# Kernel optimization log

Hardware: AMD Instinct MI355X
Metric: run time of the kernel (lower is better)

## Reference

```python
import jax, jax.numpy as jnp
import numpy as np

B, T, C, H = 2, 2048, 1024, 16
HD = C // H  # head dim = 64


def setup_inputs() -> dict:
    key = jax.random.key(0)
    ks = jax.random.split(key, 5)
    s = 0.02  # GPT-style init scale for weights
    return {
        "x": jax.random.normal(ks[0], (B, T, C), dtype=jnp.float32),
        "Wq": jax.random.normal(ks[1], (C, C), dtype=jnp.float32) * s,
        "bq": jnp.zeros((C,), dtype=jnp.float32),
        "Wk": jax.random.normal(ks[2], (C, C), dtype=jnp.float32) * s,
        "bk": jnp.zeros((C,), dtype=jnp.float32),
        "Wv": jax.random.normal(ks[3], (C, C), dtype=jnp.float32) * s,
        "bv": jnp.zeros((C,), dtype=jnp.float32),
        "Wp": jax.random.normal(ks[4], (C, C), dtype=jnp.float32) * s,
        "bp": jnp.zeros((C,), dtype=jnp.float32),
    }


def reference(x, Wq, bq, Wk, bk, Wv, bv, Wp, bp):
    b, t, c = x.shape
    # torch nn.Linear: y = x @ W.T + b  (W is [out, in])
    def heads(W, bias):
        y = jnp.einsum("btc,oc->bto", x, W) + bias
        return y.reshape(b, t, H, HD).transpose(0, 2, 1, 3)  # [B,H,T,hd]

    q = heads(Wq, bq)
    k = heads(Wk, bk)
    v = heads(Wv, bv)

    scale = 1.0 / np.sqrt(HD).astype(np.float32)
    att = jnp.einsum("bhqd,bhkd->bhqk", q, k) * scale  # [B,H,T,T]
    causal = jnp.tril(jnp.ones((t, t), dtype=bool))
    att = jnp.where(causal[None, None], att, -jnp.inf)
    att = jax.nn.softmax(att, axis=-1)
    # attn_pdrop = 0.0 -> dropout is identity
    y = jnp.einsum("bhqk,bhkd->bhqd", att, v)  # [B,H,T,hd]
    y = y.transpose(0, 2, 1, 3).reshape(b, t, c)
    y = jnp.einsum("btc,oc->bto", y, Wp) + bp  # resid_pdrop = 0.0
    return y
```

## Files before the change

kernel.cpp:

```cpp
#include <hip/hip_runtime.h>
#include <hip/hip_bf16.h>

using bf16 = __hip_bfloat16;
typedef __attribute__((ext_vector_type(8))) short short8;
typedef __attribute__((ext_vector_type(4))) float floatx4;

#define B_  2
#define T_  2048
#define C_  1024
#define H_  16
#define HD_ 64
#define BT_ (B_*T_)
#define NX_ ((size_t)BT_*C_)
#define NW_ ((size_t)C_*C_)
#define PSTR2 40
#define KSCQ 0.1803368801f

__device__ __forceinline__ void gl2lds16(const bf16* g, bf16* l) {
    __builtin_amdgcn_global_load_lds((const __attribute__((address_space(1))) unsigned int*)g,
                                     (__attribute__((address_space(3))) unsigned int*)l,
                                     16, 0, 0);
}

__global__ __launch_bounds__(256) void cvt_f32_bf16(
    const float* __restrict__ x,
    const float* __restrict__ Wq, const float* __restrict__ Wk,
    const float* __restrict__ Wv, const float* __restrict__ Wp,
    bf16* __restrict__ xb, bf16* __restrict__ wqb, bf16* __restrict__ wkb,
    bf16* __restrict__ wvb, bf16* __restrict__ wpb)
{
    size_t i4 = ((size_t)blockIdx.x * 256 + threadIdx.x) * 4;
    const float* src; bf16* dst; size_t off;
    if (i4 < NX_) { src = x; dst = xb; off = i4; }
    else {
        size_t j = i4 - NX_;
        int r = (int)(j >> 20);
        off = j & (NW_ - 1);
        src = (r==0) ? Wq : (r==1) ? Wk : (r==2) ? Wv : Wp;
        dst = (r==0) ? wqb : (r==1) ? wkb : (r==2) ? wvb : wpb;
    }
    float4 v = *(const float4*)(src + off);
    union { bf16 h[4]; uint2 u; } o;
    o.h[0] = __float2bfloat16(v.x); o.h[1] = __float2bfloat16(v.y);
    o.h[2] = __float2bfloat16(v.z); o.h[3] = __float2bfloat16(v.w);
    *(uint2*)(dst + off) = o.u;
}

__global__ __launch_bounds__(256) void qkv_gemm(
    const bf16* __restrict__ x,
    const bf16* __restrict__ Wq, const float* __restrict__ bq,
    const bf16* __restrict__ Wk, const float* __restrict__ bk,
    const bf16* __restrict__ Wv, const float* __restrict__ bv,
    bf16* __restrict__ qo, bf16* __restrict__ ko, bf16* __restrict__ vt)
{
    __shared__ __align__(16) bf16 As[128*32];
    __shared__ __align__(16) bf16 Bs[128*32];

    const int tid  = threadIdx.x;
    const int w    = tid >> 6, lane = tid & 63;
    const int g    = lane >> 4, c16 = lane & 15;
    const int wr   = w >> 1,    wc  = w & 1;
    const int mtile = blockIdx.x, ntile = blockIdx.y;
    const int wsel  = ntile >> 3;
    const bf16*  W    = (wsel==0) ? Wq : (wsel==1 ? Wk : Wv);
    const float* bias = (wsel==0) ? bq : (wsel==1 ? bk : bv);
    const float oscale = (wsel==0) ? KSCQ : 1.0f;
    const int nbase  = (ntile & 7) * 128;

    const bf16* ag = x + (size_t)(mtile*128)*C_;
    const bf16* bg = W + (size_t)nbase*C_;

    floatx4 acc[4][4] = {};

    for (int k0 = 0; k0 < C_; k0 += 32) {
        #pragma unroll
        for (int p = 0; p < 2; ++p) {
            int cb = p*256 + w*64;
            int c  = cb + lane;
            gl2lds16(ag + (size_t)(c>>2)*C_ + k0 + (c&3)*8, As + cb*8);
            gl2lds16(bg + (size_t)(c>>2)*C_ + k0 + (c&3)*8, Bs + cb*8);
        }
        __syncthreads();

        short8 af[4], bfr[4];
        #pragma unroll
        for (int i = 0; i < 4; ++i)
            af[i] = *(const short8*)(As + (wr*64 + i*16 + c16)*32 + g*8);
        #pragma unroll
        for (int j = 0; j < 4; ++j)
            bfr[j] = *(const short8*)(Bs + (wc*64 + j*16 + c16)*32 + g*8);
        #pragma unroll
        for (int i = 0; i < 4; ++i)
            #pragma unroll
            for (int j = 0; j < 4; ++j)
                acc[i][j] = __builtin_amdgcn_mfma_f32_16x16x32_bf16(af[i], bfr[j], acc[i][j], 0, 0, 0);
        __syncthreads();
    }

    #pragma unroll
    for (int i = 0; i < 4; ++i) {
        int m0 = mtile*128 + wr*64 + i*16 + g*4;
        #pragma unroll
        for (int j = 0; j < 4; ++j) {
            int n = nbase + wc*64 + j*16 + c16;
            float bvf = bias[n];
            if (wsel == 2) {
                int bb = m0 >> 11, t0 = m0 & (T_-1);
                int hh = n >> 6,  hd = n & 63;
                union { bf16 hv[4]; uint2 u; } tmp;
                #pragma unroll
                for (int r = 0; r < 4; ++r) tmp.hv[r] = __float2bfloat16(acc[i][j][r] + bvf);
                *(uint2*)(vt + ((size_t)((bb*H_ + hh)*64 + hd))*T_ + t0) = tmp.u;
            } else {
                bf16* dst = (wsel==0) ? qo : ko;
                #pragma unroll
                for (int r = 0; r < 4; ++r)
                    dst[(size_t)(m0+r)*C_ + n] = __float2bfloat16((acc[i][j][r] + bvf) * oscale);
            }
        }
    }
}

__global__ __launch_bounds__(512, 4) void attn(
    const bf16* __restrict__ q, const bf16* __restrict__ k,
    const bf16* __restrict__ vt, bf16* __restrict__ y)
{
    __shared__ __align__(16) bf16 Ks[16*512];
    __shared__ __align__(16) bf16 Vs[16*512];
    __shared__ __align__(16) bf16 Ps[8][16*PSTR2];

    const int tid = threadIdx.x, w = tid >> 6, lane = tid & 63;
    const int g = lane >> 4, c16 = lane & 15;
    const int wq = w & 3;
    const int kh = w >> 2;

    const int xcd = blockIdx.x & 7;
    const int j   = blockIdx.x >> 3;
    const int p   = j & 15;
    const int bh  = (j >> 4) * 8 + xcd;
    const int b = bh >> 4, h = bh & 15;

    const bf16* kbase = k  + ((size_t)(b*T_))*C_ + h*64;
    const bf16* vbase = vt + ((size_t)(b*H_ + h))*64*T_;

    const short ONEB = 0x3F80;
    const short8 ones = {ONEB,ONEB,ONEB,ONEB,ONEB,ONEB,ONEB,ONEB};

    for (int ph = 0; ph < 2; ++ph) {
        const int qt = ph ? 31 - p : p;
        const int qbase = qt*64 + wq*16;
        const int nit = (qt + 2) >> 1;
        const int qglob = qbase + c16;

        short8 aq[2];
        #pragma unroll
        for (int kg = 0; kg < 2; ++kg)
            aq[kg] = *(const short8*)(q + ((size_t)(b*T_ + qglob))*C_ + h*64 + kg*32 + g*8);

        floatx4 accO[4] = {};
        floatx4 lacc = {};

        for (int kt = 0; kt < nit; ++kt) {
            #pragma unroll
            for (int e = 0; e < 2; ++e) {
                int f = w*2 + e;
                gl2lds16(kbase + (size_t)(kt*128 + (f>>1)*16 + c16)*C_ + (f&1)*32 + g*8, Ks + f*512);
                gl2lds16(vbase + (size_t)((f&3)*16 + c16)*T_ + kt*128 + (f>>2)*32 + g*8, Vs + f*512);
            }
            __syncthreads();

            floatx4 s[4];
            #pragma unroll
            for (int ct = 0; ct < 4; ++ct) {
                int ce = kh*4 + ct;
                short8 kb0 = *(const short8*)(Ks + (ce*2+0)*512 + lane*8);
                short8 kb1 = *(const short8*)(Ks + (ce*2+1)*512 + lane*8);
                floatx4 a = {0.f, 0.f, 0.f, 0.f};
                a = __builtin_amdgcn_mfma_f32_16x16x32_bf16(kb0, aq[0], a, 0, 0, 0);
                a = __builtin_amdgcn_mfma_f32_16x16x32_bf16(kb1, aq[1], a, 0, 0, 0);
                s[ct] = a;
            }

            if (kt == nit-1) {
                #pragma unroll
                for (int ct = 0; ct < 4; ++ct)
                    #pragma unroll
                    for (int r = 0; r < 4; ++r) {
                        int key = kt*128 + kh*64 + ct*16 + g*4 + r;
                        if (key > qglob) s[ct][r] = -1e30f;
                    }
            }

            #pragma unroll
            for (int ks = 0; ks < 2; ++ks) {
                #pragma unroll
                for (int half = 0; half < 2; ++half) {
                    int ct = ks*2 + half;
                    float p0 = exp2f(s[ct][0]);
                    float p1 = exp2f(s[ct][1]);
                    float p2 = exp2f(s[ct][2]);
                    float p3 = exp2f(s[ct][3]);
                    union { __hip_bfloat162 h2[2]; uint2 u; } pk;
                    pk.h2[0] = __float22bfloat162_rn(float2{p0, p1});
                    pk.h2[1] = __float22bfloat162_rn(float2{p2, p3});
                    *(uint2*)(Ps[w] + c16*PSTR2 + half*16 + g*4) = pk.u;
                }
                short8 pa = *(const short8*)(Ps[w] + c16*PSTR2 + g*8);
                lacc = __builtin_amdgcn_mfma_f32_16x16x32_bf16(pa, ones, lacc, 0, 0, 0);
                #pragma unroll
                for (int nt = 0; nt < 4; ++nt) {
                    short8 vb = *(const short8*)(Vs + ((kh*2 + ks)*4 + nt)*512 + lane*8);
                    accO[nt] = __builtin_amdgcn_mfma_f32_16x16x32_bf16(pa, vb, accO[nt], 0, 0, 0);
                }
            }
            __syncthreads();
        }

        if (w >= 4) {
            float* dstf = ((w < 6) ? (float*)Ks : (float*)Vs) + (w & 1)*1280 + lane*20;
            #pragma unroll
            for (int nt = 0; nt < 4; ++nt) *(floatx4*)(dstf + nt*4) = accO[nt];
            *(floatx4*)(dstf + 16) = lacc;
        }
        __syncthreads();
        if (w < 4) {
            int pw = w + 4;
            const float* srcf = ((pw < 6) ? (const float*)Ks : (const float*)Vs) + (pw & 1)*1280 + lane*20;
            #pragma unroll
            for (int nt = 0; nt < 4; ++nt) {
                floatx4 o = *(const floatx4*)(srcf + nt*4);
                #pragma unroll
                for (int r = 0; r < 4; ++r) accO[nt][r] += o[r];
            }
            floatx4 lo = *(const floatx4*)(srcf + 16);
            #pragma unroll
            for (int r = 0; r < 4; ++r) lacc[r] += lo[r];

            float ir[4];
            #pragma unroll
            for (int r = 0; r < 4; ++r) ir[r] = __builtin_amdgcn_rcpf(lacc[r]);
            #pragma unroll
            for (int nt = 0; nt < 4; ++nt)
                #pragma unroll
                for (int r = 0; r < 4; ++r) {
                    int row = qbase + g*4 + r;
                    float o = accO[nt][r] * ir[r];
                    y[((size_t)(b*T_ + row))*C_ + h*64 + nt*16 + c16] = __float2bfloat16(o);
                }
        }
        __syncthreads();
    }
}

__global__ __launch_bounds__(256) void proj_gemm(
    const bf16* __restrict__ yin, const bf16* __restrict__ Wp, const float* __restrict__ bp,
    float* __restrict__ out)
{
    __shared__ __align__(16) bf16 As[64*32];
    __shared__ __align__(16) bf16 Bs[128*32];

    const int tid = threadIdx.x;
    const int w = tid >> 6, lane = tid & 63;
    const int g = lane >> 4, c16 = lane & 15;
    const int mtile = blockIdx.x, ntile = blockIdx.y;
    const int nbase = ntile * 128;

    const bf16* ag = yin + (size_t)(mtile*64)*C_;
    const bf16* bg = Wp  + (size_t)nbase*C_;

    floatx4 acc[4][2] = {};

    for (int k0 = 0; k0 < C_; k0 += 32) {
        gl2lds16(ag + (size_t)(w*16 + (lane>>2))*C_ + k0 + (lane&3)*8, As + w*512);
        #pragma unroll
        for (int p = 0; p < 2; ++p) {
            int cb = p*256 + w*64;
            int c  = cb + lane;
            gl2lds16(bg + (size_t)(c>>2)*C_ + k0 + (c&3)*8, Bs + cb*8);
        }
        __syncthreads();

        short8 af[4], bfr[2];
        #pragma unroll
        for (int i = 0; i < 4; ++i)
            af[i] = *(const short8*)(As + (i*16 + c16)*32 + g*8);
        #pragma unroll
        for (int j = 0; j < 2; ++j)
            bfr[j] = *(const short8*)(Bs + (w*32 + j*16 + c16)*32 + g*8);
        #pragma unroll
        for (int i = 0; i < 4; ++i)
            #pragma unroll
            for (int j = 0; j < 2; ++j)
                acc[i][j] = __builtin_amdgcn_mfma_f32_16x16x32_bf16(af[i], bfr[j], acc[i][j], 0, 0, 0);
        __syncthreads();
    }

    #pragma unroll
    for (int i = 0; i < 4; ++i) {
        int m0 = mtile*64 + i*16 + g*4;
        #pragma unroll
        for (int j = 0; j < 2; ++j) {
            int n = nbase + w*32 + j*16 + c16;
            float bvf = bp[n];
            #pragma unroll
            for (int r = 0; r < 4; ++r)
                out[(size_t)(m0+r)*C_ + n] = acc[i][j][r] + bvf;
        }
    }
}

extern "C" void kernel_launch(void* const* d_in, const int* in_sizes, int n_in,
                              void* d_out, int out_size, void* d_ws, size_t ws_size,
                              hipStream_t stream) {
    const float* x  = (const float*)d_in[0];
    const float* Wq = (const float*)d_in[1];
    const float* bq = (const float*)d_in[2];
    const float* Wk = (const float*)d_in[3];
    const float* bk = (const float*)d_in[4];
    const float* Wv = (const float*)d_in[5];
    const float* bv = (const float*)d_in[6];
    const float* Wp = (const float*)d_in[7];
    const float* bp = (const float*)d_in[8];

    bf16* xb  = (bf16*)d_ws;
    bf16* wqb = xb  + NX_;
    bf16* wkb = wqb + NW_;
    bf16* wvb = wkb + NW_;
    bf16* wpb = wvb + NW_;
    bf16* qw  = wpb + NW_;
    bf16* kw  = qw  + NX_;
    bf16* vt  = kw  + NX_;
    bf16* yw  = vt  + NX_;

    const int cvt_blocks = (int)((NX_ + 4*NW_) / (4*256));
    cvt_f32_bf16<<<cvt_blocks, 256, 0, stream>>>(x, Wq, Wk, Wv, Wp, xb, wqb, wkb, wvb, wpb);
    qkv_gemm<<<dim3(32, 24), 256, 0, stream>>>(xb, wqb, bq, wkb, bk, wvb, bv, qw, kw, vt);
    attn    <<<512, 512, 0, stream>>>(qw, kw, vt, yw);
    proj_gemm<<<dim3(64, 8), 256, 0, stream>>>(yw, wpb, bp, (float*)d_out);
}
```

Baseline: 184.2 us.

## Process paired causal query tiles together to share K/V loads in attention

Instead of running the short and long query tiles of a pair in two sequential phases that each reload K/V, the attention kernel now runs both tiles in one key loop. Each K/V tile loaded into LDS feeds both query tiles while the short tile is still active. The block-to-work mapping is also reordered so that pairs are interleaved across the grid. The cost is roughly double the accumulator registers (two sets of O and l) and an extra P buffer in LDS, which may lower occupancy under the 512-thread launch bound.

```diff
diff --git a/kernel.cpp b/kernel.cpp
--- a/kernel.cpp
+++ b/kernel.cpp
@@ -127,128 +127,191 @@
 {
     __shared__ __align__(16) bf16 Ks[16*512];
     __shared__ __align__(16) bf16 Vs[16*512];
-    __shared__ __align__(16) bf16 Ps[8][16*PSTR2];
+    __shared__ __align__(16) bf16 Ps[8][2][16*PSTR2];
 
     const int tid = threadIdx.x, w = tid >> 6, lane = tid & 63;
     const int g = lane >> 4, c16 = lane & 15;
     const int wq = w & 3;
     const int kh = w >> 2;
 
-    const int xcd = blockIdx.x & 7;
-    const int j   = blockIdx.x >> 3;
-    const int p   = j & 15;
-    const int bh  = (j >> 4) * 8 + xcd;
+    const int bid = blockIdx.x;
+    const int xcd = bid & 7;
+    const int bhh = (bid >> 3) & 3;
+    const int pp  = (bid >> 5) & 7;
+    const int hi  = bid >> 8;
+    const int p   = hi ? 15 - pp : pp;
+    const int qtA = p, qtB = 31 - p;
+    const int bh  = bhh*8 + xcd;
     const int b = bh >> 4, h = bh & 15;
+
+    const int nitA = (qtA + 2) >> 1;
+    const int nitB = (qtB + 2) >> 1;
+    const int qbaseA = qtA*64 + wq*16, qbaseB = qtB*64 + wq*16;
+    const int qglobA = qbaseA + c16,   qglobB = qbaseB + c16;
 
     const bf16* kbase = k  + ((size_t)(b*T_))*C_ + h*64;
     const bf16* vbase = vt + ((size_t)(b*H_ + h))*64*T_;
 
+    short8 aqA[2], aqB[2];
+    #pragma unroll
+    for (int kg = 0; kg < 2; ++kg) {
+        aqA[kg] = *(const short8*)(q + ((size_t)(b*T_ + qglobA))*C_ + h*64 + kg*32 + g*8);
+        aqB[kg] = *(const short8*)(q + ((size_t)(b*T_ + qglobB))*C_ + h*64 + kg*32 + g*8);
+    }
+
     const short ONEB = 0x3F80;
     const short8 ones = {ONEB,ONEB,ONEB,ONEB,ONEB,ONEB,ONEB,ONEB};
 
-    for (int ph = 0; ph < 2; ++ph) {
-        const int qt = ph ? 31 - p : p;
-        const int qbase = qt*64 + wq*16;
-        const int nit = (qt + 2) >> 1;
-        const int qglob = qbase + c16;
-
-        short8 aq[2];
-        #pragma unroll
-        for (int kg = 0; kg < 2; ++kg)
-            aq[kg] = *(const short8*)(q + ((size_t)(b*T_ + qglob))*C_ + h*64 + kg*32 + g*8);
-
-        floatx4 accO[4] = {};
-        floatx4 lacc = {};
-
-        for (int kt = 0; kt < nit; ++kt) {
-            #pragma unroll
-            for (int e = 0; e < 2; ++e) {
-                int f = w*2 + e;
-                gl2lds16(kbase + (size_t)(kt*128 + (f>>1)*16 + c16)*C_ + (f&1)*32 + g*8, Ks + f*512);
-                gl2lds16(vbase + (size_t)((f&3)*16 + c16)*T_ + kt*128 + (f>>2)*32 + g*8, Vs + f*512);
-            }
-            __syncthreads();
-
-            floatx4 s[4];
-            #pragma unroll
-            for (int ct = 0; ct < 4; ++ct) {
-                int ce = kh*4 + ct;
-                short8 kb0 = *(const short8*)(Ks + (ce*2+0)*512 + lane*8);
-                short8 kb1 = *(const short8*)(Ks + (ce*2+1)*512 + lane*8);
+    floatx4 accOA[4] = {}, accOB[4] = {};
+    floatx4 laccA = {}, laccB = {};
+
+    for (int kt = 0; kt < nitB; ++kt) {
+        const bool actA = (kt < nitA);
+        #pragma unroll
+        for (int e = 0; e < 2; ++e) {
+            int f = w*2 + e;
+            gl2lds16(kbase + (size_t)(kt*128 + (f>>1)*16 + c16)*C_ + (f&1)*32 + g*8, Ks + f*512);
+            gl2lds16(vbase + (size_t)((f&3)*16 + c16)*T_ + kt*128 + (f>>2)*32 + g*8, Vs + f*512);
+        }
+        __syncthreads();
+
+        floatx4 sA[4], sB[4];
+        #pragma unroll
+        for (int ct = 0; ct < 4; ++ct) {
+            int ce = kh*4 + ct;
+            short8 kb0 = *(const short8*)(Ks + (ce*2+0)*512 + lane*8);
+            short8 kb1 = *(const short8*)(Ks + (ce*2+1)*512 + lane*8);
+            if (actA) {
                 floatx4 a = {0.f, 0.f, 0.f, 0.f};
-                a = __builtin_amdgcn_mfma_f32_16x16x32_bf16(kb0, aq[0], a, 0, 0, 0);
-                a = __builtin_amdgcn_mfma_f32_16x16x32_bf16(kb1, aq[1], a, 0, 0, 0);
-                s[ct] = a;
-            }
-
-            if (kt == nit-1) {
-                #pragma unroll
-                for (int ct = 0; ct < 4; ++ct)
-                    #pragma unroll
-                    for (int r = 0; r < 4; ++r) {
-                        int key = kt*128 + kh*64 + ct*16 + g*4 + r;
-                        if (key > qglob) s[ct][r] = -1e30f;
-                    }
-            }
-
-            #pragma unroll
-            for (int ks = 0; ks < 2; ++ks) {
-                #pragma unroll
-                for (int half = 0; half < 2; ++half) {
-                    int ct = ks*2 + half;
-                    float p0 = exp2f(s[ct][0]);
-                    float p1 = exp2f(s[ct][1]);
-                    float p2 = exp2f(s[ct][2]);
-                    float p3 = exp2f(s[ct][3]);
+                a = __builtin_amdgcn_mfma_f32_16x16x32_bf16(kb0, aqA[0], a, 0, 0, 0);
+                a = __builtin_amdgcn_mfma_f32_16x16x32_bf16(kb1, aqA[1], a, 0, 0, 0);
+                sA[ct] = a;
+            }
+            floatx4 bacc = {0.f, 0.f, 0.f, 0.f};
+            bacc = __builtin_amdgcn_mfma_f32_16x16x32_bf16(kb0, aqB[0], bacc, 0, 0, 0);
+            bacc = __builtin_amdgcn_mfma_f32_16x16x32_bf16(kb1, aqB[1], bacc, 0, 0, 0);
+            sB[ct] = bacc;
+        }
+
+        if (actA && kt == nitA-1) {
+            #pragma unroll
+            for (int ct = 0; ct < 4; ++ct)
+                #pragma unroll
+                for (int r = 0; r < 4; ++r) {
+                    int key = kt*128 + kh*64 + ct*16 + g*4 + r;
+                    if (key > qglobA) sA[ct][r] = -1e30f;
+                }
+        }
+        if (kt == nitB-1) {
+            #pragma unroll
+            for (int ct = 0; ct < 4; ++ct)
+                #pragma unroll
+                for (int r = 0; r < 4; ++r) {
+                    int key = kt*128 + kh*64 + ct*16 + g*4 + r;
+                    if (key > qglobB) sB[ct][r] = -1e30f;
+                }
+        }
+
+        #pragma unroll
+        for (int ks = 0; ks < 2; ++ks) {
+            #pragma unroll
+            for (int half = 0; half < 2; ++half) {
+                int ct = ks*2 + half;
+                if (actA) {
                     union { __hip_bfloat162 h2[2]; uint2 u; } pk;
-                    pk.h2[0] = __float22bfloat162_rn(float2{p0, p1});
-                    pk.h2[1] = __float22bfloat162_rn(float2{p2, p3});
-                    *(uint2*)(Ps[w] + c16*PSTR2 + half*16 + g*4) = pk.u;
+                    pk.h2[0] = __float22bfloat162_rn(float2{exp2f(sA[ct][0]), exp2f(sA[ct][1])});
+                    pk.h2[1] = __float22bfloat162_rn(float2{exp2f(sA[ct][2]), exp2f(sA[ct][3])});
+                    *(uint2*)(Ps[w][0] + c16*PSTR2 + half*16 + g*4) = pk.u;
                 }
-                short8 pa = *(const short8*)(Ps[w] + c16*PSTR2 + g*8);
-                lacc = __builtin_amdgcn_mfma_f32_16x16x32_bf16(pa, ones, lacc, 0, 0, 0);
+                union { __hip_bfloat162 h2[2]; uint2 u; } pkb;
+                pkb.h2[0] = __float22bfloat162_rn(float2{exp2f(sB[ct][0]), exp2f(sB[ct][1])});
+                pkb.h2[1] = __float22bfloat162_rn(float2{exp2f(sB[ct][2]), exp2f(sB[ct][3])});
+                *(uint2*)(Ps[w][1] + c16*PSTR2 + half*16 + g*4) = pkb.u;
+            }
+            short8 paB = *(const short8*)(Ps[w][1] + c16*PSTR2 + g*8);
+            laccB = __builtin_amdgcn_mfma_f32_16x16x32_bf16(paB, ones, laccB, 0, 0, 0);
+            if (actA) {
+                short8 paA = *(const short8*)(Ps[w][0] + c16*PSTR2 + g*8);
+                laccA = __builtin_amdgcn_mfma_f32_16x16x32_bf16(paA, ones, laccA, 0, 0, 0);
                 #pragma unroll
                 for (int nt = 0; nt < 4; ++nt) {
                     short8 vb = *(const short8*)(Vs + ((kh*2 + ks)*4 + nt)*512 + lane*8);
-                    accO[nt] = __builtin_amdgcn_mfma_f32_16x16x32_bf16(pa, vb, accO[nt], 0, 0, 0);
+                    accOA[nt] = __builtin_amdgcn_mfma_f32_16x16x32_bf16(paA, vb, accOA[nt], 0, 0, 0);
+                    accOB[nt] = __builtin_amdgcn_mfma_f32_16x16x32_bf16(paB, vb, accOB[nt], 0, 0, 0);
                 }
-            }
-            __syncthreads();
-        }
-
-        if (w >= 4) {
-            float* dstf = ((w < 6) ? (float*)Ks : (float*)Vs) + (w & 1)*1280 + lane*20;
-            #pragma unroll
-            for (int nt = 0; nt < 4; ++nt) *(floatx4*)(dstf + nt*4) = accO[nt];
-            *(floatx4*)(dstf + 16) = lacc;
-        }
-        __syncthreads();
-        if (w < 4) {
-            int pw = w + 4;
-            const float* srcf = ((pw < 6) ? (const float*)Ks : (const float*)Vs) + (pw & 1)*1280 + lane*20;
-            #pragma unroll
-            for (int nt = 0; nt < 4; ++nt) {
-                floatx4 o = *(const floatx4*)(srcf + nt*4);
-                #pragma unroll
-                for (int r = 0; r < 4; ++r) accO[nt][r] += o[r];
-            }
-            floatx4 lo = *(const floatx4*)(srcf + 16);
-            #pragma unroll
-            for (int r = 0; r < 4; ++r) lacc[r] += lo[r];
-
-            float ir[4];
-            #pragma unroll
-            for (int r = 0; r < 4; ++r) ir[r] = __builtin_amdgcn_rcpf(lacc[r]);
-            #pragma unroll
-            for (int nt = 0; nt < 4; ++nt)
-                #pragma unroll
-                for (int r = 0; r < 4; ++r) {
-                    int row = qbase + g*4 + r;
-                    float o = accO[nt][r] * ir[r];
-                    y[((size_t)(b*T_ + row))*C_ + h*64 + nt*16 + c16] = __float2bfloat16(o);
+            } else {
+                #pragma unroll
+                for (int nt = 0; nt < 4; ++nt) {
+                    short8 vb = *(const short8*)(Vs + ((kh*2 + ks)*4 + nt)*512 + lane*8);
+                    accOB[nt] = __builtin_amdgcn_mfma_f32_16x16x32_bf16(paB, vb, accOB[nt], 0, 0, 0);
                 }
-        }
-        __syncthreads();
+            }
+        }
+        __syncthreads();
+    }
+
+    if (w >= 4) {
+        float* dstf = ((w < 6) ? (float*)Ks : (float*)Vs) + (w & 1)*1280 + lane*20;
+        #pragma unroll
+        for (int nt = 0; nt < 4; ++nt) *(floatx4*)(dstf + nt*4) = accOA[nt];
+        *(floatx4*)(dstf + 16) = laccA;
+    }
+    __syncthreads();
+    if (w < 4) {
+        int pw = w + 4;
+        const float* srcf = ((pw < 6) ? (const float*)Ks : (const float*)Vs) + (pw & 1)*1280 + lane*20;
+        #pragma unroll
+        for (int nt = 0; nt < 4; ++nt) {
+            floatx4 o = *(const floatx4*)(srcf + nt*4);
+            #pragma unroll
+            for (int r = 0; r < 4; ++r) accOA[nt][r] += o[r];
+        }
+        floatx4 lo = *(const floatx4*)(srcf + 16);
+        #pragma unroll
+        for (int r = 0; r < 4; ++r) laccA[r] += lo[r];
+        float ir[4];
+        #pragma unroll
+        for (int r = 0; r < 4; ++r) ir[r] = __builtin_amdgcn_rcpf(laccA[r]);
+        #pragma unroll
+        for (int nt = 0; nt < 4; ++nt)
+            #pragma unroll
+            for (int r = 0; r < 4; ++r) {
+                int row = qbaseA + g*4 + r;
+                y[((size_t)(b*T_ + row))*C_ + h*64 + nt*16 + c16] =
+                    __float2bfloat16(accOA[nt][r] * ir[r]);
+            }
+    }
+    __syncthreads();
+    if (w >= 4) {
+        float* dstf = ((w < 6) ? (float*)Ks : (float*)Vs) + (w & 1)*1280 + lane*20;
+        #pragma unroll
+        for (int nt = 0; nt < 4; ++nt) *(floatx4*)(dstf + nt*4) = accOB[nt];
+        *(floatx4*)(dstf + 16) = laccB;
+    }
+    __syncthreads();
+    if (w < 4) {
+        int pw = w + 4;
+        const float* srcf = ((pw < 6) ? (const float*)Ks : (const float*)Vs) + (pw & 1)*1280 + lane*20;
+        #pragma unroll
+        for (int nt = 0; nt < 4; ++nt) {
+            floatx4 o = *(const floatx4*)(srcf + nt*4);
+            #pragma unroll
+            for (int r = 0; r < 4; ++r) accOB[nt][r] += o[r];
+        }
+        floatx4 lo = *(const floatx4*)(srcf + 16);
+        #pragma unroll
+        for (int r = 0; r < 4; ++r) laccB[r] += lo[r];
+        float ir[4];
+        #pragma unroll
+        for (int r = 0; r < 4; ++r) ir[r] = __builtin_amdgcn_rcpf(laccB[r]);
+        #pragma unroll
+        for (int nt = 0; nt < 4; ++nt)
+            #pragma unroll
+            for (int r = 0; r < 4; ++r) {
+                int row = qbaseB + g*4 + r;
+                y[((size_t)(b*T_ + row))*C_ + h*64 + nt*16 + c16] =
+                    __float2bfloat16(accOB[nt][r] * ir[r]);
+            }
     }
 }
 
```

New measurement: 193.2 us. 4.9% more time.
